# Kernel optimization log

Measured on AMD Instinct MI355X. Metric: run time of the kernel, lower is better.

## Reference

```python
import jax, jax.numpy as jnp
import numpy as np

WS = 8            # window_size
SHIFT = WS // 2   # cyclic shift for 'SW' type
HEAD_DIM = 32

def _rel_index(ws):
    # pairwise relative coordinate indices within a window, offset to [0, 2ws-2]
    cord = np.array([[i, j] for i in range(ws) for j in range(ws)])
    rel = cord[:, None, :] - cord[None, :, :] + ws - 1
    return rel[:, :, 0], rel[:, :, 1]

def _shift_mask(h_w, w_w, p):
    # boolean attention mask for shifted windows; True = masked (-inf)
    s = p - SHIFT
    m = np.zeros((h_w, w_w, p, p, p, p), dtype=bool)
    m[-1, :, :s, :, s:, :] = True
    m[-1, :, s:, :, :s, :] = True
    m[:, -1, :, :s, :, s:] = True
    m[:, -1, :, s:, :, :s] = True
    return m.reshape(h_w * w_w, p * p, p * p)

def setup_inputs() -> dict:
    key = jax.random.key(0)
    ks = jax.random.split(key, 6)
    b, H, W, c = 4, 256, 256, 256
    nh = c // HEAD_DIM
    return {
        "x": jax.random.normal(ks[0], (b, H, W, c), jnp.float32),
        "W_qkv": jax.random.normal(ks[1], (c, 3 * c), jnp.float32) * 0.02,
        "b_qkv": jnp.zeros((3 * c,), jnp.float32),
        "rel_pos": jax.random.normal(ks[2], (nh, 2 * WS - 1, 2 * WS - 1), jnp.float32) * 0.02,
        "W_out": jax.random.normal(ks[3], (c, c), jnp.float32) * 0.02,
        "b_out": jnp.zeros((c,), jnp.float32),
    }

def reference(x, W_qkv, b_qkv, rel_pos, W_out, b_out):
    b, H, W, c = x.shape
    nh = c // HEAD_DIM
    scale = HEAD_DIM ** -0.5
    # cyclic shift (type == 'SW')
    x = jnp.roll(x, (-SHIFT, -SHIFT), axis=(1, 2))
    hw, ww = H // WS, W // WS
    nw, p2 = hw * ww, WS * WS
    # partition into windows: [b, nw, p2, c]
    xw = x.reshape(b, hw, WS, ww, WS, c).transpose(0, 1, 3, 2, 4, 5).reshape(b, nw, p2, c)
    # QKV projection; layout of out dim is (3, n_heads, head_dim)
    qkv = (xw @ W_qkv + b_qkv).reshape(b, nw, p2, 3, nh, HEAD_DIM)
    q, k, v = qkv[..., 0, :, :], qkv[..., 1, :, :], qkv[..., 2, :, :]
    # attention scores per head/window: [h, b, nw, p2, p2]
    sim = jnp.einsum('bwphc,bwqhc->hbwpq', q, k) * scale
    ri, rj = _rel_index(WS)
    sim = sim + rel_pos[:, ri, rj][:, None, None]            # relative position bias
    mask = jnp.asarray(_shift_mask(hw, ww, WS))              # [nw, p2, p2]
    sim = jnp.where(mask[None, None], -jnp.inf, sim)
    probs = jax.nn.softmax(sim, axis=-1)
    out = jnp.einsum('hbwpq,bwqhc->bwphc', probs, v).reshape(b, nw, p2, nh * HEAD_DIM)
    out = out @ W_out + b_out
    # un-window: [b, H, W, c_out]
    out = out.reshape(b, hw, ww, WS, WS, -1).transpose(0, 1, 3, 2, 4, 5).reshape(b, H, W, -1)
    return jnp.roll(out, (SHIFT, SHIFT), axis=(1, 2))
```

## Files before the change

### kernel.cpp

```cpp
#include <hip/hip_runtime.h>

typedef __attribute__((ext_vector_type(4))) float f32x4;
typedef __attribute__((ext_vector_type(8))) short s16x8;
typedef __attribute__((ext_vector_type(4))) short s16x4;
typedef __attribute__((ext_vector_type(8))) __bf16 bf16v8;

#define LDS_XS 0
#define LDS_QS 32768
#define LDS_KS 65536
#define LDS_VT 98304
#define LDS_PR 131072
#define LDS_TOT 147456

__device__ __forceinline__ f32x4 mfma16(s16x8 a, s16x8 b, f32x4 c) {
  return __builtin_amdgcn_mfma_f32_16x16x32_bf16(
      __builtin_bit_cast(bf16v8, a), __builtin_bit_cast(bf16v8, b), c, 0, 0, 0);
}

__device__ __forceinline__ short f2bf(float f) {
  unsigned u = __float_as_uint(f);
  u += 0x7fffu + ((u >> 16) & 1u);
  return (short)(u >> 16);
}
__device__ __forceinline__ float bf2f(short h) {
  return __uint_as_float(((unsigned)(unsigned short)h) << 16);
}

__device__ __forceinline__ int swz512(int row, int colByte) {
  return row * 512 + (colByte ^ ((row & 7) << 4));
}
__device__ __forceinline__ int swz128(int row, int colByte) {
  return row * 128 + (colByte ^ ((row & 7) << 4));
}

__global__ void prep_w(const float* __restrict__ Wqkv, const float* __restrict__ Wout,
                       const float* __restrict__ relp,
                       short* __restrict__ wqkvT, short* __restrict__ woutTh,
                       short* __restrict__ woutTl, float* __restrict__ relt) {
  int t = blockIdx.x * 256 + threadIdx.x;
  if (t < 768 * 256) {
    int n = t >> 8, k = t & 255;
    wqkvT[t] = f2bf(Wqkv[k * 768 + n]);
  } else if (t < 768 * 256 + 256 * 256) {
    int t2 = t - 768 * 256;
    int n = t2 >> 8, k = t2 & 255;
    float wv = Wout[k * 256 + n];
    short hi = f2bf(wv);
    woutTh[t2] = hi;
    woutTl[t2] = f2bf(wv - bf2f(hi));
  } else {
    int u = t - 768 * 256 - 256 * 256;
    int r = u & 3, l = (u >> 2) & 63, strip = (u >> 8) & 3;
    int qt = (u >> 10) & 3, h = (u >> 12) & 7, var = (u >> 15) & 3;
    int p = strip * 16 + (l & 15);
    int q = qt * 16 + ((l >> 4) << 2) + r;
    int pi = p >> 3, pj = p & 7, qi = q >> 3, qj = q & 7;
    bool mrow = (var >> 1) & 1, mcol = var & 1;
    bool mk = (mrow && ((pi < 4) != (qi < 4))) || (mcol && ((pj < 4) != (qj < 4)));
    relt[u] = mk ? -1e30f : relp[h * 225 + (pi - qi + 7) * 15 + (pj - qj + 7)];
  }
}

__global__ __launch_bounds__(512, 2) void swin_mfma(
    const float* __restrict__ x, const float* __restrict__ bqkv,
    const float* __restrict__ bout,
    const short* __restrict__ wqkvT, const short* __restrict__ woutTh,
    const short* __restrict__ woutTl, const float* __restrict__ relt,
    float* __restrict__ out)
{
  __shared__ __align__(16) char lds[LDS_TOT];

  const int tx = threadIdx.x;
  const int w  = tx >> 6;
  const int l  = tx & 63;
  const int g  = l >> 4;
  const int li = l & 15;

  const int b   = blockIdx.x >> 10;
  const int wdw = blockIdx.x & 1023;
  const int wh  = wdw >> 5, wwi = wdw & 31;

  for (int i = 0; i < 8; ++i) {
    int idx = tx + i * 512;
    int p = idx >> 6, c4 = idx & 63;
    int pi = p >> 3, pj = p & 7;
    int sr = (wh * 8 + pi + 4) & 255;
    int sc = (wwi * 8 + pj + 4) & 255;
    f32x4 v = *(const f32x4*)(x + ((((size_t)b * 256 + sr) * 256 + sc) * 256 + c4 * 4));
    s16x4 h4;
    h4.x = f2bf(v.x); h4.y = f2bf(v.y); h4.z = f2bf(v.z); h4.w = f2bf(v.w);
    *(s16x4*)(lds + LDS_XS + swz512(p, c4 * 8)) = h4;
  }
  __syncthreads();

  {
    f32x4 acc[6][4];
    #pragma unroll
    for (int j = 0; j < 6; ++j)
      #pragma unroll
      for (int rb = 0; rb < 4; ++rb)
        acc[j][rb] = (f32x4){0.f, 0.f, 0.f, 0.f};

    int ocol[6];
    #pragma unroll
    for (int j = 0; j < 4; ++j) ocol[j] = (w * 4 + j) * 16 + li;
    #pragma unroll
    for (int j = 4; j < 6; ++j) ocol[j] = 512 + (w * 2 + (j - 4)) * 16 + li;

    s16x8 bcur[6], bnext[6];
    #pragma unroll
    for (int j = 0; j < 6; ++j)
      bcur[j] = *(const s16x8*)(wqkvT + (size_t)ocol[j] * 256 + g * 8);

    #pragma unroll
    for (int kk = 0; kk < 8; ++kk) {
      s16x8 a[4];
      #pragma unroll
      for (int rb = 0; rb < 4; ++rb)
        a[rb] = *(const s16x8*)(lds + LDS_XS + swz512(rb * 16 + li, kk * 64 + g * 16));
      if (kk < 7) {
        #pragma unroll
        for (int j = 0; j < 6; ++j)
          bnext[j] = *(const s16x8*)(wqkvT + (size_t)ocol[j] * 256 + (kk + 1) * 32 + g * 8);
      }
      #pragma unroll
      for (int j = 0; j < 4; ++j)
        #pragma unroll
        for (int rb = 0; rb < 4; ++rb)
          acc[j][rb] = mfma16(bcur[j], a[rb], acc[j][rb]);
      #pragma unroll
      for (int j = 4; j < 6; ++j)
        #pragma unroll
        for (int rb = 0; rb < 4; ++rb)
          acc[j][rb] = mfma16(a[rb], bcur[j], acc[j][rb]);
      if (kk < 7) {
        #pragma unroll
        for (int j = 0; j < 6; ++j) bcur[j] = bnext[j];
      }
    }

    #pragma unroll
    for (int j = 0; j < 4; ++j) {
      const int cb = w * 4 + j;
      if (cb < 16) {
        f32x4 bq = *(const f32x4*)(bqkv + cb * 16 + g * 4);
        #pragma unroll
        for (int rb = 0; rb < 4; ++rb) {
          s16x4 pk;
          pk.x = f2bf((acc[j][rb][0] + bq[0]) * 0.17677669529663687f);
          pk.y = f2bf((acc[j][rb][1] + bq[1]) * 0.17677669529663687f);
          pk.z = f2bf((acc[j][rb][2] + bq[2]) * 0.17677669529663687f);
          pk.w = f2bf((acc[j][rb][3] + bq[3]) * 0.17677669529663687f);
          *(s16x4*)(lds + LDS_QS + swz512(rb * 16 + li, cb * 32 + g * 8)) = pk;
        }
      } else {
        f32x4 bk = *(const f32x4*)(bqkv + 256 + (cb - 16) * 16 + g * 4);
        #pragma unroll
        for (int rb = 0; rb < 4; ++rb) {
          s16x4 pk;
          pk.x = f2bf(acc[j][rb][0] + bk[0]);
          pk.y = f2bf(acc[j][rb][1] + bk[1]);
          pk.z = f2bf(acc[j][rb][2] + bk[2]);
          pk.w = f2bf(acc[j][rb][3] + bk[3]);
          *(s16x4*)(lds + LDS_KS + swz512(rb * 16 + li, (cb - 16) * 32 + g * 8)) = pk;
        }
      }
    }
    #pragma unroll
    for (int j = 4; j < 6; ++j) {
      const int d = (w * 2 + (j - 4)) * 16 + li;
      const float bv = bqkv[512 + d];
      #pragma unroll
      for (int rb = 0; rb < 4; ++rb) {
        s16x4 pk;
        pk.x = f2bf(acc[j][rb][0] + bv);
        pk.y = f2bf(acc[j][rb][1] + bv);
        pk.z = f2bf(acc[j][rb][2] + bv);
        pk.w = f2bf(acc[j][rb][3] + bv);
        *(s16x4*)(lds + LDS_VT + swz128(d, rb * 32 + g * 8)) = pk;
      }
    }
  }
  __syncthreads();

  {
    const int rvar = ((wh == 31) ? 2 : 0) | ((wwi == 31) ? 1 : 0);
    const int hsel = w >> 2, strip = w & 3, p0 = strip * 16;
    const short ONE = (short)0x3F80;
    const s16x8 ones = {ONE, ONE, ONE, ONE, ONE, ONE, ONE, ONE};

    #pragma unroll
    for (int hp = 0; hp < 4; ++hp) {
      const int h = hp * 2 + hsel;

      f32x4 rc[4];
      #pragma unroll
      for (int qt = 0; qt < 4; ++qt)
        rc[qt] = *(const f32x4*)(relt + ((((rvar * 8 + h) * 4 + qt) * 4 + strip) * 64 + l) * 4);

      s16x8 qf = *(const s16x8*)(lds + LDS_QS + swz512(p0 + li, h * 64 + g * 16));
      f32x4 simT[4];
      #pragma unroll
      for (int qt = 0; qt < 4; ++qt) {
        s16x8 kf = *(const s16x8*)(lds + LDS_KS + swz512(qt * 16 + li, h * 64 + g * 16));
        simT[qt] = mfma16(kf, qf, rc[qt]);
      }

      #pragma unroll
      for (int qt = 0; qt < 4; ++qt) {
        s16x4 pk;
        pk.x = f2bf(__expf(simT[qt][0]));
        pk.y = f2bf(__expf(simT[qt][1]));
        pk.z = f2bf(__expf(simT[qt][2]));
        pk.w = f2bf(__expf(simT[qt][3]));
        *(s16x4*)(lds + LDS_PR + hsel * 8192 + swz128(p0 + li, qt * 32 + g * 8)) = pk;
      }

      s16x8 pf[2];
      #pragma unroll
      for (int ks = 0; ks < 2; ++ks)
        pf[ks] = *(const s16x8*)(lds + LDS_PR + hsel * 8192 + swz128(p0 + li, ks * 64 + g * 16));

      f32x4 s = (f32x4){0.f, 0.f, 0.f, 0.f};
      f32x4 at0 = (f32x4){0.f, 0.f, 0.f, 0.f};
      f32x4 at1 = (f32x4){0.f, 0.f, 0.f, 0.f};
      #pragma unroll
      for (int ks = 0; ks < 2; ++ks) {
        s = mfma16(ones, pf[ks], s);
        s16x8 vf0 = *(const s16x8*)(lds + LDS_VT + swz128(h * 32 + li, ks * 64 + g * 16));
        s16x8 vf1 = *(const s16x8*)(lds + LDS_VT + swz128(h * 32 + 16 + li, ks * 64 + g * 16));
        at0 = mfma16(vf0, pf[ks], at0);
        at1 = mfma16(vf1, pf[ks], at1);
      }
      const float rinv = 1.0f / s[0];

      #pragma unroll
      for (int dt = 0; dt < 2; ++dt) {
        const f32x4 at = dt ? at1 : at0;
        s16x4 hi4, lo4;
        #pragma unroll
        for (int r = 0; r < 4; ++r) {
          float v = at[r] * rinv;
          short hi = f2bf(v);
          hi4[r] = hi;
          lo4[r] = f2bf(v - bf2f(hi));
        }
        const int cByte = h * 64 + dt * 32 + g * 8;
        *(s16x4*)(lds + LDS_QS + swz512(p0 + li, cByte)) = hi4;
        *(s16x4*)(lds + LDS_XS + swz512(p0 + li, cByte)) = lo4;
      }
    }
  }
  __syncthreads();

  {
    f32x4 acc2[2][4];
    #pragma unroll
    for (int c = 0; c < 2; ++c)
      #pragma unroll
      for (int rb = 0; rb < 4; ++rb)
        acc2[c][rb] = (f32x4){0.f, 0.f, 0.f, 0.f};

    s16x8 bhc[2], blc[2], bhn[2], bln[2];
    #pragma unroll
    for (int c = 0; c < 2; ++c) {
      const size_t base = (size_t)((w * 2 + c) * 16 + li) * 256 + g * 8;
      bhc[c] = *(const s16x8*)(woutTh + base);
      blc[c] = *(const s16x8*)(woutTl + base);
    }

    #pragma unroll
    for (int kk = 0; kk < 8; ++kk) {
      s16x8 ah[4], al[4];
      #pragma unroll
      for (int rb = 0; rb < 4; ++rb) {
        const int off = swz512(rb * 16 + li, kk * 64 + g * 16);
        ah[rb] = *(const s16x8*)(lds + LDS_QS + off);
        al[rb] = *(const s16x8*)(lds + LDS_XS + off);
      }
      if (kk < 7) {
        #pragma unroll
        for (int c = 0; c < 2; ++c) {
          const size_t base = (size_t)((w * 2 + c) * 16 + li) * 256 + (kk + 1) * 32 + g * 8;
          bhn[c] = *(const s16x8*)(woutTh + base);
          bln[c] = *(const s16x8*)(woutTl + base);
        }
      }
      #pragma unroll
      for (int c = 0; c < 2; ++c)
        #pragma unroll
        for (int rb = 0; rb < 4; ++rb) {
          acc2[c][rb] = mfma16(ah[rb], bhc[c], acc2[c][rb]);
          acc2[c][rb] = mfma16(al[rb], bhc[c], acc2[c][rb]);
          acc2[c][rb] = mfma16(ah[rb], blc[c], acc2[c][rb]);
        }
      if (kk < 7) {
        #pragma unroll
        for (int c = 0; c < 2; ++c) { bhc[c] = bhn[c]; blc[c] = bln[c]; }
      }
    }

    #pragma unroll
    for (int c = 0; c < 2; ++c) {
      const int n = (w * 2 + c) * 16 + li;
      const float bo = bout[n];
      #pragma unroll
      for (int rb = 0; rb < 4; ++rb)
        #pragma unroll
        for (int r = 0; r < 4; ++r) {
          int m = rb * 16 + g * 4 + r;
          int pi = m >> 3, pj = m & 7;
          int dr = (wh * 8 + pi + 4) & 255;
          int dc = (wwi * 8 + pj + 4) & 255;
          out[(((size_t)b * 256 + dr) * 256 + dc) * 256 + n] = acc2[c][rb][r] + bo;
        }
    }
  }
}

extern "C" void kernel_launch(void* const* d_in, const int* in_sizes, int n_in,
                              void* d_out, int out_size, void* d_ws, size_t ws_size,
                              hipStream_t stream) {
  (void)in_sizes; (void)n_in; (void)out_size; (void)ws_size;
  const float* x    = (const float*)d_in[0];
  const float* Wqkv = (const float*)d_in[1];
  const float* bqkv = (const float*)d_in[2];
  const float* relp = (const float*)d_in[3];
  const float* Wout = (const float*)d_in[4];
  const float* bout = (const float*)d_in[5];
  float* out = (float*)d_out;

  short* wqkvT  = (short*)d_ws;
  short* woutTh = wqkvT + 768 * 256;
  short* woutTl = woutTh + 256 * 256;
  float* relt   = (float*)(woutTl + 256 * 256);

  hipLaunchKernelGGL(prep_w, dim3(1536), dim3(256), 0, stream,
                     Wqkv, Wout, relp, wqkvT, woutTh, woutTl, relt);
  hipLaunchKernelGGL(swin_mfma, dim3(4096), dim3(512), 0, stream,
                     x, bqkv, bout, wqkvT, woutTh, woutTl, relt, out);
}
```

Before: 477.4 us.

## Pack bf16 conversions, pad V/P LDS rows, prefetch attention operands, retile output GEMM

Result: slower. 569.2 us (+19.2%).

```diff
diff --git a/kernel.cpp b/kernel.cpp
--- a/kernel.cpp
+++ b/kernel.cpp
@@ -1,6 +1,8 @@
 #include <hip/hip_runtime.h>
+#include <hip/hip_bf16.h>
 
 typedef __attribute__((ext_vector_type(4))) float f32x4;
+typedef __attribute__((ext_vector_type(2))) unsigned int u32x2;
 typedef __attribute__((ext_vector_type(8))) short s16x8;
 typedef __attribute__((ext_vector_type(4))) short s16x4;
 typedef __attribute__((ext_vector_type(8))) __bf16 bf16v8;
@@ -9,12 +11,21 @@
 #define LDS_QS 32768
 #define LDS_KS 65536
 #define LDS_VT 98304
-#define LDS_PR 131072
-#define LDS_TOT 147456
+#define LDS_PR 139264
+#define LDS_TOT 159744
+#define VT_STR 160
+#define PR_STR 160
 
 __device__ __forceinline__ f32x4 mfma16(s16x8 a, s16x8 b, f32x4 c) {
   return __builtin_amdgcn_mfma_f32_16x16x32_bf16(
       __builtin_bit_cast(bf16v8, a), __builtin_bit_cast(bf16v8, b), c, 0, 0, 0);
+}
+
+__device__ __forceinline__ unsigned int cvt2(float a, float b) {
+  __hip_bfloat162 r = __float22bfloat162_rn(make_float2(a, b));
+  unsigned int u;
+  __builtin_memcpy(&u, &r, 4);
+  return u;
 }
 
 __device__ __forceinline__ short f2bf(float f) {
@@ -28,9 +39,6 @@
 
 __device__ __forceinline__ int swz512(int row, int colByte) {
   return row * 512 + (colByte ^ ((row & 7) << 4));
-}
-__device__ __forceinline__ int swz128(int row, int colByte) {
-  return row * 128 + (colByte ^ ((row & 7) << 4));
 }
 
 __global__ void prep_w(const float* __restrict__ Wqkv, const float* __restrict__ Wout,
@@ -87,9 +95,10 @@
     int sr = (wh * 8 + pi + 4) & 255;
     int sc = (wwi * 8 + pj + 4) & 255;
     f32x4 v = *(const f32x4*)(x + ((((size_t)b * 256 + sr) * 256 + sc) * 256 + c4 * 4));
-    s16x4 h4;
-    h4.x = f2bf(v.x); h4.y = f2bf(v.y); h4.z = f2bf(v.z); h4.w = f2bf(v.w);
-    *(s16x4*)(lds + LDS_XS + swz512(p, c4 * 8)) = h4;
+    u32x2 uu;
+    uu.x = cvt2(v[0], v[1]);
+    uu.y = cvt2(v[2], v[3]);
+    *(u32x2*)(lds + LDS_XS + swz512(p, c4 * 8)) = uu;
   }
   __syncthreads();
 
@@ -146,23 +155,20 @@
         f32x4 bq = *(const f32x4*)(bqkv + cb * 16 + g * 4);
         #pragma unroll
         for (int rb = 0; rb < 4; ++rb) {
-          s16x4 pk;
-          pk.x = f2bf((acc[j][rb][0] + bq[0]) * 0.17677669529663687f);
-          pk.y = f2bf((acc[j][rb][1] + bq[1]) * 0.17677669529663687f);
-          pk.z = f2bf((acc[j][rb][2] + bq[2]) * 0.17677669529663687f);
-          pk.w = f2bf((acc[j][rb][3] + bq[3]) * 0.17677669529663687f);
-          *(s16x4*)(lds + LDS_QS + swz512(rb * 16 + li, cb * 32 + g * 8)) = pk;
+          const float SC = 0.17677669529663687f;
+          u32x2 uu;
+          uu.x = cvt2((acc[j][rb][0] + bq[0]) * SC, (acc[j][rb][1] + bq[1]) * SC);
+          uu.y = cvt2((acc[j][rb][2] + bq[2]) * SC, (acc[j][rb][3] + bq[3]) * SC);
+          *(u32x2*)(lds + LDS_QS + swz512(rb * 16 + li, cb * 32 + g * 8)) = uu;
         }
       } else {
         f32x4 bk = *(const f32x4*)(bqkv + 256 + (cb - 16) * 16 + g * 4);
         #pragma unroll
         for (int rb = 0; rb < 4; ++rb) {
-          s16x4 pk;
-          pk.x = f2bf(acc[j][rb][0] + bk[0]);
-          pk.y = f2bf(acc[j][rb][1] + bk[1]);
-          pk.z = f2bf(acc[j][rb][2] + bk[2]);
-          pk.w = f2bf(acc[j][rb][3] + bk[3]);
-          *(s16x4*)(lds + LDS_KS + swz512(rb * 16 + li, (cb - 16) * 32 + g * 8)) = pk;
+          u32x2 uu;
+          uu.x = cvt2(acc[j][rb][0] + bk[0], acc[j][rb][1] + bk[1]);
+          uu.y = cvt2(acc[j][rb][2] + bk[2], acc[j][rb][3] + bk[3]);
+          *(u32x2*)(lds + LDS_KS + swz512(rb * 16 + li, (cb - 16) * 32 + g * 8)) = uu;
         }
       }
     }
@@ -172,12 +178,10 @@
       const float bv = bqkv[512 + d];
       #pragma unroll
       for (int rb = 0; rb < 4; ++rb) {
-        s16x4 pk;
-        pk.x = f2bf(acc[j][rb][0] + bv);
-        pk.y = f2bf(acc[j][rb][1] + bv);
-        pk.z = f2bf(acc[j][rb][2] + bv);
-        pk.w = f2bf(acc[j][rb][3] + bv);
-        *(s16x4*)(lds + LDS_VT + swz128(d, rb * 32 + g * 8)) = pk;
+        u32x2 uu;
+        uu.x = cvt2(acc[j][rb][0] + bv, acc[j][rb][1] + bv);
+        uu.y = cvt2(acc[j][rb][2] + bv, acc[j][rb][3] + bv);
+        *(u32x2*)(lds + LDS_VT + d * VT_STR + rb * 32 + g * 8) = uu;
       }
     }
   }
@@ -188,131 +192,152 @@
     const int hsel = w >> 2, strip = w & 3, p0 = strip * 16;
     const short ONE = (short)0x3F80;
     const s16x8 ones = {ONE, ONE, ONE, ONE, ONE, ONE, ONE, ONE};
+    char* prbase = lds + LDS_PR + hsel * (64 * PR_STR);
+
+    f32x4 rcn[4];
+    #pragma unroll
+    for (int qt = 0; qt < 4; ++qt)
+      rcn[qt] = *(const f32x4*)(relt + ((((rvar * 8 + hsel) * 4 + qt) * 4 + strip) * 64 + l) * 4);
 
     #pragma unroll
     for (int hp = 0; hp < 4; ++hp) {
       const int h = hp * 2 + hsel;
-
       f32x4 rc[4];
       #pragma unroll
+      for (int qt = 0; qt < 4; ++qt) rc[qt] = rcn[qt];
+
+      s16x8 qf = *(const s16x8*)(lds + LDS_QS + swz512(p0 + li, h * 64 + g * 16));
+      s16x8 kf[4];
+      #pragma unroll
       for (int qt = 0; qt < 4; ++qt)
-        rc[qt] = *(const f32x4*)(relt + ((((rvar * 8 + h) * 4 + qt) * 4 + strip) * 64 + l) * 4);
-
-      s16x8 qf = *(const s16x8*)(lds + LDS_QS + swz512(p0 + li, h * 64 + g * 16));
+        kf[qt] = *(const s16x8*)(lds + LDS_KS + swz512(qt * 16 + li, h * 64 + g * 16));
+      s16x8 vf[2][2];
+      #pragma unroll
+      for (int ks = 0; ks < 2; ++ks)
+        #pragma unroll
+        for (int dt = 0; dt < 2; ++dt)
+          vf[ks][dt] = *(const s16x8*)(lds + LDS_VT + (h * 32 + dt * 16 + li) * VT_STR
+                                       + ks * 64 + g * 16);
+      if (hp < 3) {
+        #pragma unroll
+        for (int qt = 0; qt < 4; ++qt)
+          rcn[qt] = *(const f32x4*)(relt
+              + ((((rvar * 8 + (h + 2)) * 4 + qt) * 4 + strip) * 64 + l) * 4);
+      }
+
       f32x4 simT[4];
       #pragma unroll
+      for (int qt = 0; qt < 4; ++qt) simT[qt] = mfma16(kf[qt], qf, rc[qt]);
+
+      #pragma unroll
       for (int qt = 0; qt < 4; ++qt) {
-        s16x8 kf = *(const s16x8*)(lds + LDS_KS + swz512(qt * 16 + li, h * 64 + g * 16));
-        simT[qt] = mfma16(kf, qf, rc[qt]);
-      }
-
-      #pragma unroll
-      for (int qt = 0; qt < 4; ++qt) {
-        s16x4 pk;
-        pk.x = f2bf(__expf(simT[qt][0]));
-        pk.y = f2bf(__expf(simT[qt][1]));
-        pk.z = f2bf(__expf(simT[qt][2]));
-        pk.w = f2bf(__expf(simT[qt][3]));
-        *(s16x4*)(lds + LDS_PR + hsel * 8192 + swz128(p0 + li, qt * 32 + g * 8)) = pk;
+        u32x2 uu;
+        uu.x = cvt2(__expf(simT[qt][0]), __expf(simT[qt][1]));
+        uu.y = cvt2(__expf(simT[qt][2]), __expf(simT[qt][3]));
+        *(u32x2*)(prbase + (p0 + li) * PR_STR + qt * 32 + g * 8) = uu;
       }
 
       s16x8 pf[2];
       #pragma unroll
       for (int ks = 0; ks < 2; ++ks)
-        pf[ks] = *(const s16x8*)(lds + LDS_PR + hsel * 8192 + swz128(p0 + li, ks * 64 + g * 16));
-
+        pf[ks] = *(const s16x8*)(prbase + (p0 + li) * PR_STR + ks * 64 + g * 16);
+
+      __builtin_amdgcn_s_setprio(1);
       f32x4 s = (f32x4){0.f, 0.f, 0.f, 0.f};
       f32x4 at0 = (f32x4){0.f, 0.f, 0.f, 0.f};
       f32x4 at1 = (f32x4){0.f, 0.f, 0.f, 0.f};
       #pragma unroll
       for (int ks = 0; ks < 2; ++ks) {
-        s = mfma16(ones, pf[ks], s);
-        s16x8 vf0 = *(const s16x8*)(lds + LDS_VT + swz128(h * 32 + li, ks * 64 + g * 16));
-        s16x8 vf1 = *(const s16x8*)(lds + LDS_VT + swz128(h * 32 + 16 + li, ks * 64 + g * 16));
-        at0 = mfma16(vf0, pf[ks], at0);
-        at1 = mfma16(vf1, pf[ks], at1);
-      }
+        s   = mfma16(ones, pf[ks], s);
+        at0 = mfma16(vf[ks][0], pf[ks], at0);
+        at1 = mfma16(vf[ks][1], pf[ks], at1);
+      }
+      __builtin_amdgcn_s_setprio(0);
       const float rinv = 1.0f / s[0];
 
       #pragma unroll
       for (int dt = 0; dt < 2; ++dt) {
         const f32x4 at = dt ? at1 : at0;
-        s16x4 hi4, lo4;
-        #pragma unroll
-        for (int r = 0; r < 4; ++r) {
-          float v = at[r] * rinv;
-          short hi = f2bf(v);
-          hi4[r] = hi;
-          lo4[r] = f2bf(v - bf2f(hi));
-        }
+        float v0 = at[0] * rinv, v1 = at[1] * rinv;
+        float v2 = at[2] * rinv, v3 = at[3] * rinv;
+        unsigned int uh0 = cvt2(v0, v1), uh1 = cvt2(v2, v3);
+        float l0 = v0 - __uint_as_float(uh0 << 16);
+        float l1 = v1 - __uint_as_float(uh0 & 0xffff0000u);
+        float l2 = v2 - __uint_as_float(uh1 << 16);
+        float l3 = v3 - __uint_as_float(uh1 & 0xffff0000u);
+        u32x2 hh, ll;
+        hh.x = uh0; hh.y = uh1;
+        ll.x = cvt2(l0, l1); ll.y = cvt2(l2, l3);
         const int cByte = h * 64 + dt * 32 + g * 8;
-        *(s16x4*)(lds + LDS_QS + swz512(p0 + li, cByte)) = hi4;
-        *(s16x4*)(lds + LDS_XS + swz512(p0 + li, cByte)) = lo4;
+        *(u32x2*)(lds + LDS_QS + swz512(p0 + li, cByte)) = hh;
+        *(u32x2*)(lds + LDS_XS + swz512(p0 + li, cByte)) = ll;
       }
     }
   }
   __syncthreads();
 
   {
-    f32x4 acc2[2][4];
-    #pragma unroll
-    for (int c = 0; c < 2; ++c)
-      #pragma unroll
-      for (int rb = 0; rb < 4; ++rb)
-        acc2[c][rb] = (f32x4){0.f, 0.f, 0.f, 0.f};
-
-    s16x8 bhc[2], blc[2], bhn[2], bln[2];
-    #pragma unroll
-    for (int c = 0; c < 2; ++c) {
-      const size_t base = (size_t)((w * 2 + c) * 16 + li) * 256 + g * 8;
+    const int rr = w >> 2;
+    const int cc = w & 3;
+    f32x4 acc2[4][2];
+    #pragma unroll
+    for (int c = 0; c < 4; ++c)
+      #pragma unroll
+      for (int rb2 = 0; rb2 < 2; ++rb2)
+        acc2[c][rb2] = (f32x4){0.f, 0.f, 0.f, 0.f};
+
+    s16x8 bhc[4], blc[4], bhn[4], bln[4];
+    #pragma unroll
+    for (int c = 0; c < 4; ++c) {
+      const size_t base = (size_t)((cc * 4 + c) * 16 + li) * 256 + g * 8;
       bhc[c] = *(const s16x8*)(woutTh + base);
       blc[c] = *(const s16x8*)(woutTl + base);
     }
 
     #pragma unroll
     for (int kk = 0; kk < 8; ++kk) {
-      s16x8 ah[4], al[4];
-      #pragma unroll
-      for (int rb = 0; rb < 4; ++rb) {
-        const int off = swz512(rb * 16 + li, kk * 64 + g * 16);
-        ah[rb] = *(const s16x8*)(lds + LDS_QS + off);
-        al[rb] = *(const s16x8*)(lds + LDS_XS + off);
+      s16x8 ah[2], al[2];
+      #pragma unroll
+      for (int rb2 = 0; rb2 < 2; ++rb2) {
+        const int off = swz512((rr * 2 + rb2) * 16 + li, kk * 64 + g * 16);
+        ah[rb2] = *(const s16x8*)(lds + LDS_QS + off);
+        al[rb2] = *(const s16x8*)(lds + LDS_XS + off);
       }
       if (kk < 7) {
         #pragma unroll
-        for (int c = 0; c < 2; ++c) {
-          const size_t base = (size_t)((w * 2 + c) * 16 + li) * 256 + (kk + 1) * 32 + g * 8;
+        for (int c = 0; c < 4; ++c) {
+          const size_t base = (size_t)((cc * 4 + c) * 16 + li) * 256 + (kk + 1) * 32 + g * 8;
           bhn[c] = *(const s16x8*)(woutTh + base);
           bln[c] = *(const s16x8*)(woutTl + base);
         }
       }
       #pragma unroll
-      for (int c = 0; c < 2; ++c)
-        #pragma unroll
-        for (int rb = 0; rb < 4; ++rb) {
-          acc2[c][rb] = mfma16(ah[rb], bhc[c], acc2[c][rb]);
-          acc2[c][rb] = mfma16(al[rb], bhc[c], acc2[c][rb]);
-          acc2[c][rb] = mfma16(ah[rb], blc[c], acc2[c][rb]);
+      for (int c = 0; c < 4; ++c)
+        #pragma unroll
+        for (int rb2 = 0; rb2 < 2; ++rb2) {
+          acc2[c][rb2] = mfma16(ah[rb2], bhc[c], acc2[c][rb2]);
+          acc2[c][rb2] = mfma16(al[rb2], bhc[c], acc2[c][rb2]);
+          acc2[c][rb2] = mfma16(ah[rb2], blc[c], acc2[c][rb2]);
         }
       if (kk < 7) {
         #pragma unroll
-        for (int c = 0; c < 2; ++c) { bhc[c] = bhn[c]; blc[c] = bln[c]; }
-      }
-    }
-
-    #pragma unroll
-    for (int c = 0; c < 2; ++c) {
-      const int n = (w * 2 + c) * 16 + li;
+        for (int c = 0; c < 4; ++c) { bhc[c] = bhn[c]; blc[c] = bln[c]; }
+      }
+    }
+
+    #pragma unroll
+    for (int c = 0; c < 4; ++c) {
+      const int n = (cc * 4 + c) * 16 + li;
       const float bo = bout[n];
       #pragma unroll
-      for (int rb = 0; rb < 4; ++rb)
+      for (int rb2 = 0; rb2 < 2; ++rb2)
         #pragma unroll
         for (int r = 0; r < 4; ++r) {
-          int m = rb * 16 + g * 4 + r;
+          int m = (rr * 2 + rb2) * 16 + g * 4 + r;
           int pi = m >> 3, pj = m & 7;
           int dr = (wh * 8 + pi + 4) & 255;
           int dc = (wwi * 8 + pj + 4) & 255;
-          out[(((size_t)b * 256 + dr) * 256 + dc) * 256 + n] = acc2[c][rb][r] + bo;
+          out[(((size_t)b * 256 + dr) * 256 + dc) * 256 + n] = acc2[c][rb2][r] + bo;
         }
     }
   }
```

## Replace split-bf16 output projection with single fp16 MFMA and packed bf16 conversions

Applied to the files above, without the earlier changes.

Result: faster. 408.6 us (-14.4%).

```diff
diff --git a/kernel.cpp b/kernel.cpp
--- a/kernel.cpp
+++ b/kernel.cpp
@@ -1,9 +1,11 @@
 #include <hip/hip_runtime.h>
+#include <hip/hip_bf16.h>
 
 typedef __attribute__((ext_vector_type(4))) float f32x4;
+typedef __attribute__((ext_vector_type(2))) unsigned int u32x2;
 typedef __attribute__((ext_vector_type(8))) short s16x8;
-typedef __attribute__((ext_vector_type(4))) short s16x4;
 typedef __attribute__((ext_vector_type(8))) __bf16 bf16v8;
+typedef __attribute__((ext_vector_type(8))) _Float16 f16v8;
 
 #define LDS_XS 0
 #define LDS_QS 32768
@@ -16,15 +18,29 @@
   return __builtin_amdgcn_mfma_f32_16x16x32_bf16(
       __builtin_bit_cast(bf16v8, a), __builtin_bit_cast(bf16v8, b), c, 0, 0, 0);
 }
+__device__ __forceinline__ f32x4 mfma16h(s16x8 a, s16x8 b, f32x4 c) {
+  return __builtin_amdgcn_mfma_f32_16x16x32_f16(
+      __builtin_bit_cast(f16v8, a), __builtin_bit_cast(f16v8, b), c, 0, 0, 0);
+}
+
+__device__ __forceinline__ unsigned int cvt2(float a, float b) {
+  __hip_bfloat162 r = __float22bfloat162_rn(make_float2(a, b));
+  unsigned int u;
+  __builtin_memcpy(&u, &r, 4);
+  return u;
+}
+__device__ __forceinline__ unsigned int cvt2h(float a, float b) {
+  auto r = __builtin_amdgcn_cvt_pkrtz(a, b);
+  unsigned int u;
+  __builtin_memcpy(&u, &r, 4);
+  return u;
+}
 
 __device__ __forceinline__ short f2bf(float f) {
   unsigned u = __float_as_uint(f);
   u += 0x7fffu + ((u >> 16) & 1u);
   return (short)(u >> 16);
 }
-__device__ __forceinline__ float bf2f(short h) {
-  return __uint_as_float(((unsigned)(unsigned short)h) << 16);
-}
 
 __device__ __forceinline__ int swz512(int row, int colByte) {
   return row * 512 + (colByte ^ ((row & 7) << 4));
@@ -35,8 +51,8 @@
 
 __global__ void prep_w(const float* __restrict__ Wqkv, const float* __restrict__ Wout,
                        const float* __restrict__ relp,
-                       short* __restrict__ wqkvT, short* __restrict__ woutTh,
-                       short* __restrict__ woutTl, float* __restrict__ relt) {
+                       short* __restrict__ wqkvT, short* __restrict__ wH,
+                       float* __restrict__ relt) {
   int t = blockIdx.x * 256 + threadIdx.x;
   if (t < 768 * 256) {
     int n = t >> 8, k = t & 255;
@@ -44,10 +60,10 @@
   } else if (t < 768 * 256 + 256 * 256) {
     int t2 = t - 768 * 256;
     int n = t2 >> 8, k = t2 & 255;
-    float wv = Wout[k * 256 + n];
-    short hi = f2bf(wv);
-    woutTh[t2] = hi;
-    woutTl[t2] = f2bf(wv - bf2f(hi));
+    _Float16 h = (_Float16)Wout[k * 256 + n];
+    unsigned short us;
+    __builtin_memcpy(&us, &h, 2);
+    wH[t2] = (short)us;
   } else {
     int u = t - 768 * 256 - 256 * 256;
     int r = u & 3, l = (u >> 2) & 63, strip = (u >> 8) & 3;
@@ -64,9 +80,8 @@
 __global__ __launch_bounds__(512, 2) void swin_mfma(
     const float* __restrict__ x, const float* __restrict__ bqkv,
     const float* __restrict__ bout,
-    const short* __restrict__ wqkvT, const short* __restrict__ woutTh,
-    const short* __restrict__ woutTl, const float* __restrict__ relt,
-    float* __restrict__ out)
+    const short* __restrict__ wqkvT, const short* __restrict__ wH,
+    const float* __restrict__ relt, float* __restrict__ out)
 {
   __shared__ __align__(16) char lds[LDS_TOT];
 
@@ -87,9 +102,10 @@
     int sr = (wh * 8 + pi + 4) & 255;
     int sc = (wwi * 8 + pj + 4) & 255;
     f32x4 v = *(const f32x4*)(x + ((((size_t)b * 256 + sr) * 256 + sc) * 256 + c4 * 4));
-    s16x4 h4;
-    h4.x = f2bf(v.x); h4.y = f2bf(v.y); h4.z = f2bf(v.z); h4.w = f2bf(v.w);
-    *(s16x4*)(lds + LDS_XS + swz512(p, c4 * 8)) = h4;
+    u32x2 uu;
+    uu.x = cvt2(v[0], v[1]);
+    uu.y = cvt2(v[2], v[3]);
+    *(u32x2*)(lds + LDS_XS + swz512(p, c4 * 8)) = uu;
   }
   __syncthreads();
 
@@ -146,23 +162,20 @@
         f32x4 bq = *(const f32x4*)(bqkv + cb * 16 + g * 4);
         #pragma unroll
         for (int rb = 0; rb < 4; ++rb) {
-          s16x4 pk;
-          pk.x = f2bf((acc[j][rb][0] + bq[0]) * 0.17677669529663687f);
-          pk.y = f2bf((acc[j][rb][1] + bq[1]) * 0.17677669529663687f);
-          pk.z = f2bf((acc[j][rb][2] + bq[2]) * 0.17677669529663687f);
-          pk.w = f2bf((acc[j][rb][3] + bq[3]) * 0.17677669529663687f);
-          *(s16x4*)(lds + LDS_QS + swz512(rb * 16 + li, cb * 32 + g * 8)) = pk;
+          const float SC = 0.17677669529663687f;
+          u32x2 uu;
+          uu.x = cvt2((acc[j][rb][0] + bq[0]) * SC, (acc[j][rb][1] + bq[1]) * SC);
+          uu.y = cvt2((acc[j][rb][2] + bq[2]) * SC, (acc[j][rb][3] + bq[3]) * SC);
+          *(u32x2*)(lds + LDS_QS + swz512(rb * 16 + li, cb * 32 + g * 8)) = uu;
         }
       } else {
         f32x4 bk = *(const f32x4*)(bqkv + 256 + (cb - 16) * 16 + g * 4);
         #pragma unroll
         for (int rb = 0; rb < 4; ++rb) {
-          s16x4 pk;
-          pk.x = f2bf(acc[j][rb][0] + bk[0]);
-          pk.y = f2bf(acc[j][rb][1] + bk[1]);
-          pk.z = f2bf(acc[j][rb][2] + bk[2]);
-          pk.w = f2bf(acc[j][rb][3] + bk[3]);
-          *(s16x4*)(lds + LDS_KS + swz512(rb * 16 + li, (cb - 16) * 32 + g * 8)) = pk;
+          u32x2 uu;
+          uu.x = cvt2(acc[j][rb][0] + bk[0], acc[j][rb][1] + bk[1]);
+          uu.y = cvt2(acc[j][rb][2] + bk[2], acc[j][rb][3] + bk[3]);
+          *(u32x2*)(lds + LDS_KS + swz512(rb * 16 + li, (cb - 16) * 32 + g * 8)) = uu;
         }
       }
     }
@@ -172,12 +185,10 @@
       const float bv = bqkv[512 + d];
       #pragma unroll
       for (int rb = 0; rb < 4; ++rb) {
-        s16x4 pk;
-        pk.x = f2bf(acc[j][rb][0] + bv);
-        pk.y = f2bf(acc[j][rb][1] + bv);
-        pk.z = f2bf(acc[j][rb][2] + bv);
-        pk.w = f2bf(acc[j][rb][3] + bv);
-        *(s16x4*)(lds + LDS_VT + swz128(d, rb * 32 + g * 8)) = pk;
+        u32x2 uu;
+        uu.x = cvt2(acc[j][rb][0] + bv, acc[j][rb][1] + bv);
+        uu.y = cvt2(acc[j][rb][2] + bv, acc[j][rb][3] + bv);
+        *(u32x2*)(lds + LDS_VT + swz128(d, rb * 32 + g * 8)) = uu;
       }
     }
   }
@@ -188,6 +199,7 @@
     const int hsel = w >> 2, strip = w & 3, p0 = strip * 16;
     const short ONE = (short)0x3F80;
     const s16x8 ones = {ONE, ONE, ONE, ONE, ONE, ONE, ONE, ONE};
+    char* prbase = lds + LDS_PR + hsel * 8192;
 
     #pragma unroll
     for (int hp = 0; hp < 4; ++hp) {
@@ -208,18 +220,16 @@
 
       #pragma unroll
       for (int qt = 0; qt < 4; ++qt) {
-        s16x4 pk;
-        pk.x = f2bf(__expf(simT[qt][0]));
-        pk.y = f2bf(__expf(simT[qt][1]));
-        pk.z = f2bf(__expf(simT[qt][2]));
-        pk.w = f2bf(__expf(simT[qt][3]));
-        *(s16x4*)(lds + LDS_PR + hsel * 8192 + swz128(p0 + li, qt * 32 + g * 8)) = pk;
+        u32x2 uu;
+        uu.x = cvt2(__expf(simT[qt][0]), __expf(simT[qt][1]));
+        uu.y = cvt2(__expf(simT[qt][2]), __expf(simT[qt][3]));
+        *(u32x2*)(prbase + swz128(p0 + li, qt * 32 + g * 8)) = uu;
       }
 
       s16x8 pf[2];
       #pragma unroll
       for (int ks = 0; ks < 2; ++ks)
-        pf[ks] = *(const s16x8*)(lds + LDS_PR + hsel * 8192 + swz128(p0 + li, ks * 64 + g * 16));
+        pf[ks] = *(const s16x8*)(prbase + swz128(p0 + li, ks * 64 + g * 16));
 
       f32x4 s = (f32x4){0.f, 0.f, 0.f, 0.f};
       f32x4 at0 = (f32x4){0.f, 0.f, 0.f, 0.f};
@@ -237,17 +247,10 @@
       #pragma unroll
       for (int dt = 0; dt < 2; ++dt) {
         const f32x4 at = dt ? at1 : at0;
-        s16x4 hi4, lo4;
-        #pragma unroll
-        for (int r = 0; r < 4; ++r) {
-          float v = at[r] * rinv;
-          short hi = f2bf(v);
-          hi4[r] = hi;
-          lo4[r] = f2bf(v - bf2f(hi));
-        }
-        const int cByte = h * 64 + dt * 32 + g * 8;
-        *(s16x4*)(lds + LDS_QS + swz512(p0 + li, cByte)) = hi4;
-        *(s16x4*)(lds + LDS_XS + swz512(p0 + li, cByte)) = lo4;
+        u32x2 hh;
+        hh.x = cvt2h(at[0] * rinv, at[1] * rinv);
+        hh.y = cvt2h(at[2] * rinv, at[3] * rinv);
+        *(u32x2*)(lds + LDS_XS + swz512(p0 + li, h * 64 + dt * 32 + g * 8)) = hh;
       }
     }
   }
@@ -261,42 +264,31 @@
       for (int rb = 0; rb < 4; ++rb)
         acc2[c][rb] = (f32x4){0.f, 0.f, 0.f, 0.f};
 
-    s16x8 bhc[2], blc[2], bhn[2], bln[2];
-    #pragma unroll
-    for (int c = 0; c < 2; ++c) {
-      const size_t base = (size_t)((w * 2 + c) * 16 + li) * 256 + g * 8;
-      bhc[c] = *(const s16x8*)(woutTh + base);
-      blc[c] = *(const s16x8*)(woutTl + base);
-    }
+    s16x8 bc[2], bn[2];
+    #pragma unroll
+    for (int c = 0; c < 2; ++c)
+      bc[c] = *(const s16x8*)(wH + (size_t)((w * 2 + c) * 16 + li) * 256 + g * 8);
 
     #pragma unroll
     for (int kk = 0; kk < 8; ++kk) {
-      s16x8 ah[4], al[4];
-      #pragma unroll
-      for (int rb = 0; rb < 4; ++rb) {
-        const int off = swz512(rb * 16 + li, kk * 64 + g * 16);
-        ah[rb] = *(const s16x8*)(lds + LDS_QS + off);
-        al[rb] = *(const s16x8*)(lds + LDS_XS + off);
-      }
+      s16x8 a[4];
+      #pragma unroll
+      for (int rb = 0; rb < 4; ++rb)
+        a[rb] = *(const s16x8*)(lds + LDS_XS + swz512(rb * 16 + li, kk * 64 + g * 16));
       if (kk < 7) {
         #pragma unroll
-        for (int c = 0; c < 2; ++c) {
-          const size_t base = (size_t)((w * 2 + c) * 16 + li) * 256 + (kk + 1) * 32 + g * 8;
-          bhn[c] = *(const s16x8*)(woutTh + base);
-          bln[c] = *(const s16x8*)(woutTl + base);
-        }
+        for (int c = 0; c < 2; ++c)
+          bn[c] = *(const s16x8*)(wH + (size_t)((w * 2 + c) * 16 + li) * 256
+                                  + (kk + 1) * 32 + g * 8);
       }
       #pragma unroll
       for (int c = 0; c < 2; ++c)
         #pragma unroll
-        for (int rb = 0; rb < 4; ++rb) {
-          acc2[c][rb] = mfma16(ah[rb], bhc[c], acc2[c][rb]);
-          acc2[c][rb] = mfma16(al[rb], bhc[c], acc2[c][rb]);
-          acc2[c][rb] = mfma16(ah[rb], blc[c], acc2[c][rb]);
-        }
+        for (int rb = 0; rb < 4; ++rb)
+          acc2[c][rb] = mfma16h(a[rb], bc[c], acc2[c][rb]);
       if (kk < 7) {
         #pragma unroll
-        for (int c = 0; c < 2; ++c) { bhc[c] = bhn[c]; blc[c] = bln[c]; }
+        for (int c = 0; c < 2; ++c) bc[c] = bn[c];
       }
     }
 
@@ -330,13 +322,12 @@
   const float* bout = (const float*)d_in[5];
   float* out = (float*)d_out;
 
-  short* wqkvT  = (short*)d_ws;
-  short* woutTh = wqkvT + 768 * 256;
-  short* woutTl = woutTh + 256 * 256;
-  float* relt   = (float*)(woutTl + 256 * 256);
+  short* wqkvT = (short*)d_ws;
+  short* wH    = wqkvT + 768 * 256;
+  float* relt  = (float*)(wH + 256 * 256);
 
   hipLaunchKernelGGL(prep_w, dim3(1536), dim3(256), 0, stream,
-                     Wqkv, Wout, relp, wqkvT, woutTh, woutTl, relt);
+                     Wqkv, Wout, relp, wqkvT, wH, relt);
   hipLaunchKernelGGL(swin_mfma, dim3(4096), dim3(512), 0, stream,
-                     x, bqkv, bout, wqkvT, woutTh, woutTl, relt, out);
-}
+                     x, bqkv, bout, wqkvT, wH, relt, out);
+}
```
